# Kernel optimization log

Hardware: AMD Instinct MI355X
Metric: run time of the kernel (lower is better)

The kernel has to match this reference:

```python
import jax, jax.numpy as jnp
import numpy as np


def setup_inputs() -> dict:
    key = jax.random.key(0)
    k1, k2, k3 = jax.random.split(key, 3)
    B, L, H, E = 2, 2048, 16, 64
    queries = jax.random.normal(k1, (B, L, H, E), dtype=jnp.float32)
    keys = jax.random.normal(k2, (B, L, H, E), dtype=jnp.float32)
    values = jax.random.normal(k3, (B, L, H, E), dtype=jnp.float32)
    a1 = jnp.ones((), dtype=jnp.float32)
    a2 = jnp.ones((), dtype=jnp.float32)
    return {"queries": queries, "keys": keys, "values": values, "a1": a1, "a2": a2}


def reference(queries, keys, values, a1, a2):
    # ASSAAttention forward (eval mode: dropout is identity)
    B, L, H, E = queries.shape
    scale = 1.0 / jnp.sqrt(jnp.asarray(E, queries.dtype))
    # shared QK scores: [B, H, L, S]
    qk_scores = jnp.einsum('blhe,bshe->bhls', queries, keys) * scale
    # sparse path: squared-ReLU weighting
    ssa_scores = jax.nn.relu(qk_scores) ** 2
    ssa_output = jnp.einsum('bhls,bshd->blhd', ssa_scores, values)
    # dense path: softmax weighting
    dsa_scores = jax.nn.softmax(qk_scores, axis=-1)
    dsa_output = jnp.einsum('bhls,bshd->blhd', dsa_scores, values)
    # scalar blend with softmax over (a1, a2)
    w1 = jnp.exp(a1)
    w2 = jnp.exp(a2)
    alpha1 = w1 / (w1 + w2)
    alpha2 = w2 / (w1 + w2)
    return alpha1 * ssa_output + alpha2 * dsa_output
```

## Files before the change

kernel.cpp:

```cpp
#include <hip/hip_runtime.h>
#include <hip/hip_bf16.h>

typedef __attribute__((ext_vector_type(8))) short short8;
typedef __attribute__((ext_vector_type(4))) float f32x4;
typedef __attribute__((ext_vector_type(4))) unsigned uint4v;

#define LOG2E 1.4426950408889634f
#define ILN2SQ 0.4804530139182014f

__device__ __forceinline__ unsigned packbf2(float a, float b) {
  __hip_bfloat162 h = __float22bfloat162_rn(make_float2(a, b));
  return *reinterpret_cast<unsigned*>(&h);
}
__device__ __forceinline__ int swz(int row) {
  return ((row & 7) << 4) ^ (((row >> 3) & 3) << 5);
}
__device__ __forceinline__ void gload16(const void* g, void* l) {
  __builtin_amdgcn_global_load_lds(
      (const __attribute__((address_space(1))) unsigned int*)g,
      (__attribute__((address_space(3))) unsigned int*)l, 16, 0, 0);
}

__device__ __forceinline__ int pv_key(int p) {
  const int R = p >> 5, g = (p & 31) >> 3, jj = p & 7;
  return (R * 2 + (jj >> 2)) * 16 + g * 4 + (jj & 3);
}

__global__ __launch_bounds__(256) void assa_prep(
    const float* __restrict__ K, const float* __restrict__ V, char* __restrict__ WS)
{
  constexpr int L = 2048, RS = 1024, E = 64;
  char* KP = WS;
  char* VTP = WS + (size_t)8 * 1024 * 1024;
  __shared__ float tile[64][65];
  const int tid = threadIdx.x;

  if (blockIdx.x < 1024) {
    const int gid = blockIdx.x * 256 + tid;
    const int rid = gid >> 2;
    const int e0 = (gid & 3) * 16;
    const int bh = rid >> 11, s = rid & 2047;
    const int b = bh >> 4, h = bh & 15;
    const float* kr = K + ((size_t)b * L + s) * RS + h * E + e0;
    const float4 u0 = *(const float4*)(kr);
    const float4 u1 = *(const float4*)(kr + 4);
    const float4 u2 = *(const float4*)(kr + 8);
    const float4 u3 = *(const float4*)(kr + 12);
    uint4v w0, w1;
    w0[0] = packbf2(u0.x, u0.y); w0[1] = packbf2(u0.z, u0.w);
    w0[2] = packbf2(u1.x, u1.y); w0[3] = packbf2(u1.z, u1.w);
    w1[0] = packbf2(u2.x, u2.y); w1[1] = packbf2(u2.z, u2.w);
    w1[2] = packbf2(u3.x, u3.y); w1[3] = packbf2(u3.z, u3.w);
    char* dst = KP + (size_t)rid * 128;
    const int sz = swz(s);
    *(uint4v*)(dst + ((e0 * 2) ^ sz)) = w0;
    *(uint4v*)(dst + ((e0 * 2 + 16) ^ sz)) = w1;
  } else {
    const int bx = blockIdx.x - 1024;
    const int bh = bx >> 5, t5 = bx & 31;
    const int b = bh >> 4, h = bh & 15;
    const float* vb = V + ((size_t)b * L + t5 * 64) * RS + h * E;
    {
      const int key = tid >> 2, e0 = (tid & 3) * 16;
      const float* vr = vb + (size_t)key * RS + e0;
      const float4 u0 = *(const float4*)(vr);
      const float4 u1 = *(const float4*)(vr + 4);
      const float4 u2 = *(const float4*)(vr + 8);
      const float4 u3 = *(const float4*)(vr + 12);
      float* tr = &tile[key][e0];
      tr[0] = u0.x; tr[1] = u0.y; tr[2] = u0.z; tr[3] = u0.w;
      tr[4] = u1.x; tr[5] = u1.y; tr[6] = u1.z; tr[7] = u1.w;
      tr[8] = u2.x; tr[9] = u2.y; tr[10] = u2.z; tr[11] = u2.w;
      tr[12] = u3.x; tr[13] = u3.y; tr[14] = u3.z; tr[15] = u3.w;
    }
    __syncthreads();
    const int e = tid >> 2, p0 = (tid & 3) * 16;
    uint4v w0, w1;
    #pragma unroll
    for (int i = 0; i < 4; ++i)
      w0[i] = packbf2(tile[pv_key(p0 + 2 * i)][e], tile[pv_key(p0 + 2 * i + 1)][e]);
    #pragma unroll
    for (int i = 0; i < 4; ++i)
      w1[i] = packbf2(tile[pv_key(p0 + 8 + 2 * i)][e], tile[pv_key(p0 + 9 + 2 * i)][e]);
    char* dst = VTP + ((size_t)bx * 64 + e) * 128;
    const int sz = swz(e);
    *(uint4v*)(dst + ((p0 * 2) ^ sz)) = w0;
    *(uint4v*)(dst + ((p0 * 2 + 16) ^ sz)) = w1;
  }
}

__global__ __launch_bounds__(256, 2) void assa_fused(
    const float* __restrict__ Q, const char* __restrict__ WS,
    const float* __restrict__ A1, const float* __restrict__ A2,
    float* __restrict__ O)
{
  constexpr int L = 2048, H = 16, E = 64, RS = H * E;

  __shared__ __align__(16) char Kb[2 * 8192];
  __shared__ __align__(16) char Vb[2 * 8192];

  const int t = threadIdx.x;
  const int wv = t >> 6;
  const int lane = t & 63;
  const int g = lane >> 4;
  const int c = lane & 15;

  const int bh = blockIdx.x;
  const int q0 = blockIdx.y * 128;
  const int b = bh >> 4;
  const int h = bh & 15;

  const float* qb = Q + (size_t)b * L * RS + (size_t)h * E;
  float* ob = O + (size_t)b * L * RS + (size_t)h * E;
  const char* KP = WS;
  const char* VTP = WS + (size_t)8 * 1024 * 1024;

  const float a1 = A1[0], a2 = A2[0];
  const float am = fmaxf(a1, a2);
  const float e1 = expf(a1 - am), e2 = expf(a2 - am);
  const float alpha1 = (e1 / (e1 + e2)) * ILN2SQ;
  const float alpha2 = e2 / (e1 + e2);

  short8 aqA[2], aqB[2];
  {
    const float qs = 0.125f * LOG2E;
    #pragma unroll
    for (int setb = 0; setb < 2; ++setb) {
      const float* qr = qb + (size_t)(q0 + wv * 32 + setb * 16 + c) * RS;
      #pragma unroll
      for (int ks = 0; ks < 2; ++ks) {
        const float4 u0 = *(const float4*)(qr + ks * 32 + g * 8);
        const float4 u1 = *(const float4*)(qr + ks * 32 + g * 8 + 4);
        union { unsigned u[4]; short8 s; } f;
        f.u[0] = packbf2(u0.x * qs, u0.y * qs);
        f.u[1] = packbf2(u0.z * qs, u0.w * qs);
        f.u[2] = packbf2(u1.x * qs, u1.y * qs);
        f.u[3] = packbf2(u1.z * qs, u1.w * qs);
        if (setb) aqB[ks] = f.s; else aqA[ks] = f.s;
      }
    }
  }

  int ka[8];
  #pragma unroll
  for (int kt = 0; kt < 4; ++kt) {
    const int row = kt * 16 + c;
    const int s = swz(row);
    ka[kt * 2 + 0] = (row * 128 + g * 16) ^ s;
    ka[kt * 2 + 1] = (row * 128 + 64 + g * 16) ^ s;
  }
  int va[8];
  #pragma unroll
  for (int et = 0; et < 4; ++et) {
    const int row = et * 16 + c;
    const int s = swz(row);
    va[et * 2 + 0] = (row * 128 + g * 16) ^ s;
    va[et * 2 + 1] = (row * 128 + 64 + g * 16) ^ s;
  }

  const f32x4 zero4 = {0.0f, 0.0f, 0.0f, 0.0f};
  f32x4 odA[4], osA[4], odB[4], osB[4];
  #pragma unroll
  for (int i = 0; i < 4; ++i) { odA[i] = zero4; osA[i] = zero4; odB[i] = zero4; osB[i] = zero4; }
  float psumA = 0.0f, psumB = 0.0f;

  const char* kp = KP + (size_t)bh * (2048 * 128) + wv * 1024 + lane * 16;
  const char* vp = VTP + (size_t)bh * (2048 * 128) + wv * 1024 + lane * 16;
  char* kd = Kb + wv * 1024;
  char* vd = Vb + wv * 1024;

  union U8 { unsigned u[4]; short8 s; };

#define STAGE(TOFF, HALF)                              \
  do {                                                 \
    gload16(kp + (TOFF), kd + (HALF));                 \
    gload16(kp + (TOFF) + 4096, kd + (HALF) + 4096);   \
    gload16(vp + (TOFF), vd + (HALF));                 \
    gload16(vp + (TOFF) + 4096, vd + (HALF) + 4096);   \
  } while (0)

#define PROC(ACC, OD, OS, PSUM)                                                      \
  do {                                                                               \
    unsigned pdw[8], psw[8];                                                         \
    _Pragma("unroll")                                                                \
    for (int kt = 0; kt < 4; ++kt) {                                                 \
      const float x0 = __builtin_amdgcn_exp2f(ACC[kt][0]);                           \
      const float x1 = __builtin_amdgcn_exp2f(ACC[kt][1]);                           \
      const float x2 = __builtin_amdgcn_exp2f(ACC[kt][2]);                           \
      const float x3 = __builtin_amdgcn_exp2f(ACC[kt][3]);                           \
      PSUM += (x0 + x1) + (x2 + x3);                                                 \
      const float r0 = fmaxf(ACC[kt][0], 0.0f), r1 = fmaxf(ACC[kt][1], 0.0f);        \
      const float r2 = fmaxf(ACC[kt][2], 0.0f), r3 = fmaxf(ACC[kt][3], 0.0f);        \
      pdw[kt * 2 + 0] = packbf2(x0, x1);                                             \
      pdw[kt * 2 + 1] = packbf2(x2, x3);                                             \
      psw[kt * 2 + 0] = packbf2(r0 * r0, r1 * r1);                                   \
      psw[kt * 2 + 1] = packbf2(r2 * r2, r3 * r3);                                   \
    }                                                                                \
    _Pragma("unroll")                                                                \
    for (int tp = 0; tp < 2; ++tp) {                                                 \
      U8 bpd, bps;                                                                   \
      bpd.u[0] = pdw[tp * 4 + 0]; bpd.u[1] = pdw[tp * 4 + 1];                        \
      bpd.u[2] = pdw[tp * 4 + 2]; bpd.u[3] = pdw[tp * 4 + 3];                        \
      bps.u[0] = psw[tp * 4 + 0]; bps.u[1] = psw[tp * 4 + 1];                        \
      bps.u[2] = psw[tp * 4 + 2]; bps.u[3] = psw[tp * 4 + 3];                        \
      _Pragma("unroll")                                                              \
      for (int et = 0; et < 4; ++et) {                                               \
        const short8 vf = tp ? vfr1[et] : vfr0[et];                                  \
        OD[et] = __builtin_amdgcn_mfma_f32_16x16x32_bf16(vf, bpd.s, OD[et], 0, 0, 0);\
        OS[et] = __builtin_amdgcn_mfma_f32_16x16x32_bf16(vf, bps.s, OS[et], 0, 0, 0);\
      }                                                                              \
    }                                                                                \
  } while (0)

#define COMPUTE(OFS)                                                                 \
  do {                                                                               \
    f32x4 aA[4], aB[4];                                                              \
    _Pragma("unroll")                                                                \
    for (int i = 0; i < 4; ++i) { aA[i] = zero4; aB[i] = zero4; }                    \
    _Pragma("unroll")                                                                \
    for (int kt = 0; kt < 4; ++kt) {                                                 \
      const short8 kf0 = *(const short8*)(Kb + ka[kt * 2 + 0] + (OFS));              \
      const short8 kf1 = *(const short8*)(Kb + ka[kt * 2 + 1] + (OFS));              \
      aA[kt] = __builtin_amdgcn_mfma_f32_16x16x32_bf16(kf0, aqA[0], aA[kt], 0, 0, 0);\
      aA[kt] = __builtin_amdgcn_mfma_f32_16x16x32_bf16(kf1, aqA[1], aA[kt], 0, 0, 0);\
      aB[kt] = __builtin_amdgcn_mfma_f32_16x16x32_bf16(kf0, aqB[0], aB[kt], 0, 0, 0);\
      aB[kt] = __builtin_amdgcn_mfma_f32_16x16x32_bf16(kf1, aqB[1], aB[kt], 0, 0, 0);\
    }                                                                                \
    short8 vfr0[4], vfr1[4];                                                         \
    _Pragma("unroll")                                                                \
    for (int et = 0; et < 4; ++et) {                                                 \
      vfr0[et] = *(const short8*)(Vb + va[et * 2 + 0] + (OFS));                      \
      vfr1[et] = *(const short8*)(Vb + va[et * 2 + 1] + (OFS));                      \
    }                                                                                \
    PROC(aA, odA, osA, psumA);                                                       \
    PROC(aB, odB, osB, psumB);                                                       \
  } while (0)

  STAGE(0, 0);
  __syncthreads();
  size_t toff = 8192;
  for (int it = 0; it < 32; it += 2) {
    STAGE(toff, 8192); toff += 8192;
    COMPUTE(0);
    __syncthreads();
    if (it + 2 < 32) { STAGE(toff, 0); toff += 8192; }
    COMPUTE(8192);
    __syncthreads();
  }
#undef STAGE
#undef PROC
#undef COMPUTE

  float lA = psumA;
  lA += __shfl_xor(lA, 16);
  lA += __shfl_xor(lA, 32);
  float lB = psumB;
  lB += __shfl_xor(lB, 16);
  lB += __shfl_xor(lB, 32);

  const float wdA = alpha2 / lA;
  const float wdB = alpha2 / lB;
  float* orowA = ob + (size_t)(q0 + wv * 32 + c) * RS;
  float* orowB = orowA + (size_t)16 * RS;
  #pragma unroll
  for (int et = 0; et < 4; ++et) {
    float4 oa, obv;
    oa.x = alpha1 * osA[et][0] + wdA * odA[et][0];
    oa.y = alpha1 * osA[et][1] + wdA * odA[et][1];
    oa.z = alpha1 * osA[et][2] + wdA * odA[et][2];
    oa.w = alpha1 * osA[et][3] + wdA * odA[et][3];
    obv.x = alpha1 * osB[et][0] + wdB * odB[et][0];
    obv.y = alpha1 * osB[et][1] + wdB * odB[et][1];
    obv.z = alpha1 * osB[et][2] + wdB * odB[et][2];
    obv.w = alpha1 * osB[et][3] + wdB * odB[et][3];
    *(float4*)(orowA + et * 16 + g * 4) = oa;
    *(float4*)(orowB + et * 16 + g * 4) = obv;
  }
}

extern "C" void kernel_launch(void* const* d_in, const int* in_sizes, int n_in,
                              void* d_out, int out_size, void* d_ws, size_t ws_size,
                              hipStream_t stream) {
  const float* q = (const float*)d_in[0];
  const float* k = (const float*)d_in[1];
  const float* v = (const float*)d_in[2];
  const float* a1 = (const float*)d_in[3];
  const float* a2 = (const float*)d_in[4];
  float* out = (float*)d_out;
  char* ws = (char*)d_ws;

  assa_prep<<<2048, 256, 0, stream>>>(k, v, ws);
  dim3 grid(32, 16);
  assa_fused<<<grid, 256, 0, stream>>>(q, ws, a1, a2, out);
}
```

Measured before the change: 78.33 us.

## Use 512-thread blocks with 16 query rows per wave

Each block grows from 4 to 8 waves, and each wave now handles 16 query rows instead of 32, so every wave keeps one set of accumulators instead of two. The K/V staging is spread over twice as many threads, with one 16-byte load per thread per tensor. The aim is to lower register pressure and raise occupancy, at the cost of each wave re-reading K/V fragments from LDS for fewer query rows, which doubles LDS read traffic per unit of work. Barriers now also synchronize more waves.

```diff
diff --git a/kernel.cpp b/kernel.cpp
--- a/kernel.cpp
+++ b/kernel.cpp
@@ -89,7 +89,7 @@
   }
 }
 
-__global__ __launch_bounds__(256, 2) void assa_fused(
+__global__ __launch_bounds__(512, 4) void assa_fused(
     const float* __restrict__ Q, const char* __restrict__ WS,
     const float* __restrict__ A1, const float* __restrict__ A2,
     float* __restrict__ O)
@@ -121,23 +121,20 @@
   const float alpha1 = (e1 / (e1 + e2)) * ILN2SQ;
   const float alpha2 = e2 / (e1 + e2);
 
-  short8 aqA[2], aqB[2];
+  short8 aq[2];
   {
     const float qs = 0.125f * LOG2E;
+    const float* qr = qb + (size_t)(q0 + wv * 16 + c) * RS;
     #pragma unroll
-    for (int setb = 0; setb < 2; ++setb) {
-      const float* qr = qb + (size_t)(q0 + wv * 32 + setb * 16 + c) * RS;
-      #pragma unroll
-      for (int ks = 0; ks < 2; ++ks) {
-        const float4 u0 = *(const float4*)(qr + ks * 32 + g * 8);
-        const float4 u1 = *(const float4*)(qr + ks * 32 + g * 8 + 4);
-        union { unsigned u[4]; short8 s; } f;
-        f.u[0] = packbf2(u0.x * qs, u0.y * qs);
-        f.u[1] = packbf2(u0.z * qs, u0.w * qs);
-        f.u[2] = packbf2(u1.x * qs, u1.y * qs);
-        f.u[3] = packbf2(u1.z * qs, u1.w * qs);
-        if (setb) aqB[ks] = f.s; else aqA[ks] = f.s;
-      }
+    for (int ks = 0; ks < 2; ++ks) {
+      const float4 u0 = *(const float4*)(qr + ks * 32 + g * 8);
+      const float4 u1 = *(const float4*)(qr + ks * 32 + g * 8 + 4);
+      union { unsigned u[4]; short8 s; } f;
+      f.u[0] = packbf2(u0.x * qs, u0.y * qs);
+      f.u[1] = packbf2(u0.z * qs, u0.w * qs);
+      f.u[2] = packbf2(u1.x * qs, u1.y * qs);
+      f.u[3] = packbf2(u1.z * qs, u1.w * qs);
+      aq[ks] = f.s;
     }
   }
 
@@ -159,24 +156,22 @@
   }
 
   const f32x4 zero4 = {0.0f, 0.0f, 0.0f, 0.0f};
-  f32x4 odA[4], osA[4], odB[4], osB[4];
-  #pragma unroll
-  for (int i = 0; i < 4; ++i) { odA[i] = zero4; osA[i] = zero4; odB[i] = zero4; osB[i] = zero4; }
-  float psumA = 0.0f, psumB = 0.0f;
-
-  const char* kp = KP + (size_t)bh * (2048 * 128) + wv * 1024 + lane * 16;
-  const char* vp = VTP + (size_t)bh * (2048 * 128) + wv * 1024 + lane * 16;
-  char* kd = Kb + wv * 1024;
-  char* vd = Vb + wv * 1024;
+  f32x4 od[4], os[4];
+  #pragma unroll
+  for (int i = 0; i < 4; ++i) { od[i] = zero4; os[i] = zero4; }
+  float psum = 0.0f;
+
+  const char* kp = KP + (size_t)bh * (2048 * 128) + t * 16;
+  const char* vp = VTP + (size_t)bh * (2048 * 128) + t * 16;
+  char* kd = Kb + wv * 1024 + lane * 16 - lane * 16;
+  char* vd = Vb + wv * 1024 + lane * 16 - lane * 16;
 
   union U8 { unsigned u[4]; short8 s; };
 
 #define STAGE(TOFF, HALF)                              \
   do {                                                 \
     gload16(kp + (TOFF), kd + (HALF));                 \
-    gload16(kp + (TOFF) + 4096, kd + (HALF) + 4096);   \
     gload16(vp + (TOFF), vd + (HALF));                 \
-    gload16(vp + (TOFF) + 4096, vd + (HALF) + 4096);   \
   } while (0)
 
 #define PROC(ACC, OD, OS, PSUM)                                                      \
@@ -214,17 +209,15 @@
 
 #define COMPUTE(OFS)                                                                 \
   do {                                                                               \
-    f32x4 aA[4], aB[4];                                                              \
-    _Pragma("unroll")                                                                \
-    for (int i = 0; i < 4; ++i) { aA[i] = zero4; aB[i] = zero4; }                    \
+    f32x4 acc[4];                                                                    \
+    _Pragma("unroll")                                                                \
+    for (int i = 0; i < 4; ++i) acc[i] = zero4;                                      \
     _Pragma("unroll")                                                                \
     for (int kt = 0; kt < 4; ++kt) {                                                 \
       const short8 kf0 = *(const short8*)(Kb + ka[kt * 2 + 0] + (OFS));              \
       const short8 kf1 = *(const short8*)(Kb + ka[kt * 2 + 1] + (OFS));              \
-      aA[kt] = __builtin_amdgcn_mfma_f32_16x16x32_bf16(kf0, aqA[0], aA[kt], 0, 0, 0);\
-      aA[kt] = __builtin_amdgcn_mfma_f32_16x16x32_bf16(kf1, aqA[1], aA[kt], 0, 0, 0);\
-      aB[kt] = __builtin_amdgcn_mfma_f32_16x16x32_bf16(kf0, aqB[0], aB[kt], 0, 0, 0);\
-      aB[kt] = __builtin_amdgcn_mfma_f32_16x16x32_bf16(kf1, aqB[1], aB[kt], 0, 0, 0);\
+      acc[kt] = __builtin_amdgcn_mfma_f32_16x16x32_bf16(kf0, aq[0], acc[kt], 0, 0, 0);\
+      acc[kt] = __builtin_amdgcn_mfma_f32_16x16x32_bf16(kf1, aq[1], acc[kt], 0, 0, 0);\
     }                                                                                \
     short8 vfr0[4], vfr1[4];                                                         \
     _Pragma("unroll")                                                                \
@@ -232,8 +225,7 @@
       vfr0[et] = *(const short8*)(Vb + va[et * 2 + 0] + (OFS));                      \
       vfr1[et] = *(const short8*)(Vb + va[et * 2 + 1] + (OFS));                      \
     }                                                                                \
-    PROC(aA, odA, osA, psumA);                                                       \
-    PROC(aB, odB, osB, psumB);                                                       \
+    PROC(acc, od, os, psum);                                                         \
   } while (0)
 
   STAGE(0, 0);
@@ -251,30 +243,20 @@
 #undef PROC
 #undef COMPUTE
 
-  float lA = psumA;
-  lA += __shfl_xor(lA, 16);
-  lA += __shfl_xor(lA, 32);
-  float lB = psumB;
-  lB += __shfl_xor(lB, 16);
-  lB += __shfl_xor(lB, 32);
-
-  const float wdA = alpha2 / lA;
-  const float wdB = alpha2 / lB;
-  float* orowA = ob + (size_t)(q0 + wv * 32 + c) * RS;
-  float* orowB = orowA + (size_t)16 * RS;
+  float l = psum;
+  l += __shfl_xor(l, 16);
+  l += __shfl_xor(l, 32);
+
+  const float wd = alpha2 / l;
+  float* orow = ob + (size_t)(q0 + wv * 16 + c) * RS;
   #pragma unroll
   for (int et = 0; et < 4; ++et) {
-    float4 oa, obv;
-    oa.x = alpha1 * osA[et][0] + wdA * odA[et][0];
-    oa.y = alpha1 * osA[et][1] + wdA * odA[et][1];
-    oa.z = alpha1 * osA[et][2] + wdA * odA[et][2];
-    oa.w = alpha1 * osA[et][3] + wdA * odA[et][3];
-    obv.x = alpha1 * osB[et][0] + wdB * odB[et][0];
-    obv.y = alpha1 * osB[et][1] + wdB * odB[et][1];
-    obv.z = alpha1 * osB[et][2] + wdB * odB[et][2];
-    obv.w = alpha1 * osB[et][3] + wdB * odB[et][3];
-    *(float4*)(orowA + et * 16 + g * 4) = oa;
-    *(float4*)(orowB + et * 16 + g * 4) = obv;
+    float4 o;
+    o.x = alpha1 * os[et][0] + wd * od[et][0];
+    o.y = alpha1 * os[et][1] + wd * od[et][1];
+    o.z = alpha1 * os[et][2] + wd * od[et][2];
+    o.w = alpha1 * os[et][3] + wd * od[et][3];
+    *(float4*)(orow + et * 16 + g * 4) = o;
   }
 }
 
@@ -291,5 +273,5 @@
 
   assa_prep<<<2048, 256, 0, stream>>>(k, v, ws);
   dim3 grid(32, 16);
-  assa_fused<<<grid, 256, 0, stream>>>(q, ws, a1, a2, out);
-}
+  assa_fused<<<grid, 512, 0, stream>>>(q, ws, a1, a2, out);
+}
```

New measurement: 77.17 us. About the same (-1.5%).
